# Performance work log

Hardware: AMD Instinct MI355X
Metric: run time of the kernel (lower is better)

The kernel has to match this reference:

```python
import jax, jax.numpy as jnp
import numpy as np

# ---- fixed sizes ----
N_IN = 100_000          # total inner nodes
NODES_PER_INNER = 50    # nodes per inner graph
N_OUT = N_IN // NODES_PER_INNER          # 2000 outer nodes (= num inner graphs)
NODES_PER_OUTER = 125   # outer nodes per outer graph
B = N_OUT // NODES_PER_OUTER             # 16 graphs in the batch
DEG = 8
E_IN = N_IN * DEG        # 800_000 inner edges
E_OUT = N_OUT * DEG      # 16_000 outer edges
IN_FEATS = 64
OUT_FEATS = 64
H = 128                  # h_feats = [128]*6
NUM_CLASSES = 10


def _rand_edges(key, n_graphs, nodes_per_graph, edges_per_graph):
    """Random edges that stay inside each graph of a batched graph."""
    k1, k2 = jax.random.split(key)
    src_l = jax.random.randint(k1, (n_graphs, edges_per_graph), 0, nodes_per_graph)
    dst_l = jax.random.randint(k2, (n_graphs, edges_per_graph), 0, nodes_per_graph)
    off = (jnp.arange(n_graphs) * nodes_per_graph)[:, None]
    return ((src_l + off).reshape(-1).astype(jnp.int32),
            (dst_l + off).reshape(-1).astype(jnp.int32))


def setup_inputs() -> dict:
    key = jax.random.key(0)
    ks = jax.random.split(key, 24)
    inner_src, inner_dst = _rand_edges(ks[0], N_OUT, NODES_PER_INNER, E_IN // N_OUT)
    outer_src, outer_dst = _rand_edges(ks[1], B, NODES_PER_OUTER, E_OUT // B)

    def w(k, fan_in, fan_out):
        return jax.random.normal(k, (fan_in, fan_out), jnp.float32) * (1.0 / np.sqrt(fan_in))

    inp = {
        "in_layer_feat": jax.random.normal(ks[2], (N_IN, IN_FEATS), jnp.float32),
        "out_layer_feat": jax.random.normal(ks[3], (N_OUT, OUT_FEATS), jnp.float32),
        "inner_ew": jax.random.uniform(ks[4], (E_IN,), jnp.float32) + 0.5,
        "outer_ew": jax.random.uniform(ks[5], (E_OUT,), jnp.float32) + 0.5,
        "W1": w(ks[6], IN_FEATS, H),        "b1": jnp.zeros((H,), jnp.float32),
        "W2": w(ks[7], H, H),               "b2": jnp.zeros((H,), jnp.float32),
        "W3": w(ks[8], OUT_FEATS + H, H),   "b3": jnp.zeros((H,), jnp.float32),
        "W4": w(ks[9], H, H),               "b4": jnp.zeros((H,), jnp.float32),
        "W5": w(ks[10], H, H),              "b5": jnp.zeros((H,), jnp.float32),
        "W6": w(ks[11], H, H),              "b6": jnp.zeros((H,), jnp.float32),
        "Wc": w(ks[12], H, NUM_CLASSES),    "bc": jnp.zeros((NUM_CLASSES,), jnp.float32),
        "inner_src": inner_src, "inner_dst": inner_dst,
        "outer_src": outer_src, "outer_dst": outer_dst,
        "inner_node_graph": (jnp.arange(N_IN) // NODES_PER_INNER).astype(jnp.int32),
        "outer_node_graph": (jnp.arange(N_OUT) // NODES_PER_OUTER).astype(jnp.int32),
    }
    return inp


def graph_conv(src, dst, ew, x, W, b, n_nodes):
    """DGL GraphConv, norm='both', weighted aggregation, zero-in-degree allowed."""
    ones = jnp.ones(src.shape[0], x.dtype)
    deg_out = jnp.clip(jax.ops.segment_sum(ones, src, num_segments=n_nodes), 1.0)
    deg_in = jnp.clip(jax.ops.segment_sum(ones, dst, num_segments=n_nodes), 1.0)
    xs = x * jax.lax.rsqrt(deg_out)[:, None]                      # src normalization
    msg = xs[src] * ew[:, None]                                   # u_mul_e
    agg = jax.ops.segment_sum(msg, dst, num_segments=n_nodes)     # copy_e -> sum
    agg = agg * jax.lax.rsqrt(deg_in)[:, None]                    # dst normalization
    return agg @ W + b


def mean_nodes(h, node_graph, n_graphs, nodes_per_graph):
    return jax.ops.segment_sum(h, node_graph, num_segments=n_graphs) / nodes_per_graph


def reference(in_layer_feat, out_layer_feat, inner_ew, outer_ew,
              W1, b1, W2, b2, W3, b3, W4, b4, W5, b5, W6, b6, Wc, bc,
              inner_src, inner_dst, outer_src, outer_dst,
              inner_node_graph, outer_node_graph):
    # inner-graph message passing
    h = jax.nn.relu(graph_conv(inner_src, inner_dst, inner_ew, in_layer_feat, W1, b1, N_IN))
    h = jax.nn.relu(graph_conv(inner_src, inner_dst, inner_ew, h, W2, b2, N_IN))
    reduced = mean_nodes(h, inner_node_graph, N_OUT, float(NODES_PER_INNER))  # [N_OUT, H]
    merged = jnp.concatenate([out_layer_feat, reduced], axis=-1)              # [N_OUT, OUT_FEATS+H]
    # outer-graph message passing
    h = jax.nn.relu(graph_conv(outer_src, outer_dst, outer_ew, merged, W3, b3, N_OUT))
    h = jax.nn.relu(graph_conv(outer_src, outer_dst, outer_ew, h, W4, b4, N_OUT))
    h = jax.nn.relu(graph_conv(outer_src, outer_dst, outer_ew, h, W5, b5, N_OUT))
    h = jax.nn.relu(graph_conv(outer_src, outer_dst, outer_ew, h, W6, b6, N_OUT))
    hg = mean_nodes(h, outer_node_graph, B, float(NODES_PER_OUTER))           # [B, H]
    return hg @ Wc + bc                                                       # [B, NUM_CLASSES]
```

## Files before the change

kernel.cpp:

```cpp
#include <hip/hip_runtime.h>

#define NPI 50
#define EPI 400
#define NPO 125
#define EPO 1000
#define N_IN 100000
#define N_OUT 2000
#define NB 16
#define NC 10

typedef _Float16 half_t;
typedef _Float16 f16x8 __attribute__((ext_vector_type(8)));
typedef float f32x4 __attribute__((ext_vector_type(4)));

#define MFMA(a, b, c) __builtin_amdgcn_mfma_f32_16x16x32_f16(a, b, c, 0, 0, 0)

__device__ __forceinline__ f16x8 lds_ld8(const half_t* base, int row, int k, int strideB) {
    return *(const f16x8*)((const char*)base + row * strideB + ((k * 2) ^ ((row & 7) << 4)));
}
__device__ __forceinline__ void lds_st1(half_t* base, int row, int col, int strideB, float v) {
    *(half_t*)((char*)base + row * strideB + ((col * 2) ^ ((row & 7) << 4))) = (half_t)v;
}
__device__ __forceinline__ void lds_st1h(half_t* base, int row, int col, int strideB, half_t v) {
    *(half_t*)((char*)base + row * strideB + ((col * 2) ^ ((row & 7) << 4))) = v;
}
__device__ __forceinline__ void lds_st8(half_t* base, int row, int k, int strideB, f16x8 v) {
    *(f16x8*)((char*)base + row * strideB + ((k * 2) ^ ((row & 7) << 4))) = v;
}
__device__ __forceinline__ f16x8 scr_ld8(const half_t* base, int row, int k) {
    return *(const f16x8*)((const char*)base + row * 64 + ((k * 2) ^ ((row & 3) << 4)));
}
__device__ __forceinline__ void scr_st1(half_t* base, int row, int col, float v) {
    *(half_t*)((char*)base + row * 64 + ((col * 2) ^ ((row & 3) << 4))) = (half_t)v;
}

__global__ __launch_bounds__(256) void k_pre(
    const float* __restrict__ W1, const float* __restrict__ W2,
    const float* __restrict__ W3, const float* __restrict__ W4,
    const float* __restrict__ W5, const float* __restrict__ W6,
    half_t* __restrict__ WT1, half_t* __restrict__ WT2,
    half_t* __restrict__ WT3, half_t* __restrict__ WT4,
    half_t* __restrict__ WT5, half_t* __restrict__ WT6,
    const float* __restrict__ ew, const int* __restrict__ esrc,
    const int* __restrict__ edst, half_t* __restrict__ Aout)
{
    __shared__ float Af[NPO * NPO];
    __shared__ int cO[NPO], cI[NPO];
    __shared__ float rso[NPO], rsi[NPO];
    const int t = threadIdx.x;

    if (blockIdx.x < 384) {
        int i = blockIdx.x * 256 + t;
        const float* src; half_t* dst; int K;
        if      (i < 8192)  { src = W1; dst = WT1; K = 64; }
        else if (i < 24576) { src = W2; dst = WT2; K = 128; i -= 8192; }
        else if (i < 49152) { src = W3; dst = WT3; K = 192; i -= 24576; }
        else if (i < 65536) { src = W4; dst = WT4; K = 128; i -= 49152; }
        else if (i < 81920) { src = W5; dst = WT5; K = 128; i -= 65536; }
        else                { src = W6; dst = WT6; K = 128; i -= 81920; }
        int c = i & 127, k = i >> 7;
        dst[c * K + k] = (half_t)src[k * 128 + c];
        return;
    }

    const int g = blockIdx.x - 384;
    const int nb = g * NPO, eb = g * EPO;
    for (int i = t; i < NPO * NPO; i += 256) Af[i] = 0.f;
    if (t < NPO) { cO[t] = 0; cI[t] = 0; }
    __syncthreads();
    for (int e = t; e < EPO; e += 256) {
        int s = esrc[eb + e] - nb, d = edst[eb + e] - nb;
        atomicAdd(&Af[d * NPO + s], ew[eb + e]);
        atomicAdd(&cO[s], 1); atomicAdd(&cI[d], 1);
    }
    __syncthreads();
    if (t < NPO) {
        rso[t] = rsqrtf((float)max(cO[t], 1));
        rsi[t] = rsqrtf((float)max(cI[t], 1));
    }
    __syncthreads();
    for (int i = t; i < 128 * 16; i += 256) {
        int d = i >> 4, s0 = (i & 15) * 8;
        f16x8 v;
        #pragma unroll
        for (int j = 0; j < 8; j++) {
            int s = s0 + j;
            float x = (d < NPO && s < NPO) ? Af[d * NPO + s] * rsi[d] * rso[s] : 0.f;
            v[j] = (half_t)x;
        }
        *(f16x8*)&Aout[(size_t)g * 16384 + d * 128 + s0] = v;
    }
}

__global__ __launch_bounds__(256, 7) void k_inner(
    const float* __restrict__ X, const float* __restrict__ outfeat,
    const float* __restrict__ ew, const int* __restrict__ esrc,
    const int* __restrict__ edst,
    const half_t* __restrict__ WT1, const float* __restrict__ b1,
    const half_t* __restrict__ WT2, const float* __restrict__ b2,
    half_t* __restrict__ merged)
{
    __shared__ alignas(16) char smem[21504];
    half_t* R2  = (half_t*)smem;
    float*  Af  = (float*)smem;
    half_t* scr = (half_t*)(smem + 16384);
    float*  pool= (float*)(smem + 20480);
    int*    cO  = (int*)(smem + 20992);
    int*    cI  = (int*)(smem + 21248);

    const int g = blockIdx.x, t = threadIdx.x;
    const int w = t >> 6, l = t & 63, lr = l & 15, lk = l >> 4;
    const int nb = g * NPI, eb = g * EPI;
    half_t* scrw = scr + w * 512;

    float ofv = (t < 64) ? outfeat[(size_t)g * 64 + t] : 0.f;
    int s0e, d0e; float w0e;
    { int e = eb + t; s0e = esrc[e] - nb; d0e = edst[e] - nb; w0e = ew[e]; }
    int s1e = 0, d1e = 0; float w1e = 0.f;
    const bool e1v = (t + 256 < EPI);
    if (e1v) { int e = eb + t + 256; s1e = esrc[e] - nb; d1e = edst[e] - nb; w1e = ew[e]; }
    const int srow = t >> 2, qc = t & 3;
    float4 xr0 = {0,0,0,0}, xr1 = xr0, xr2 = xr0, xr3 = xr0;
    if (srow < NPI) {
        const float* xp = &X[(size_t)(nb + srow) * 64 + qc * 16];
        xr0 = *(const float4*)(xp + 0);
        xr1 = *(const float4*)(xp + 4);
        xr2 = *(const float4*)(xp + 8);
        xr3 = *(const float4*)(xp + 12);
    }

    if (t < 64) { cO[t] = 0; cI[t] = 0; }
    if (t >= 64 && t < 192) pool[t - 64] = 0.f;
    for (int i = t; i < 4096; i += 256) Af[i] = 0.f;
    __syncthreads();

    atomicAdd(&Af[d0e * 64 + (s0e ^ ((d0e & 7) << 2))], w0e);
    atomicAdd(&cO[s0e], 1); atomicAdd(&cI[d0e], 1);
    if (e1v) {
        atomicAdd(&Af[d1e * 64 + (s1e ^ ((d1e & 7) << 2))], w1e);
        atomicAdd(&cO[s1e], 1); atomicAdd(&cI[d1e], 1);
    }
    __syncthreads();

    f16x8 afr[2];
    {
        const int r = w * 16 + lr;
        const int sw = (r & 7) << 2;
        const float rsi_l = rsqrtf((float)max(cI[r], 1));
        #pragma unroll
        for (int ks = 0; ks < 2; ks++) {
            const int c0 = ks * 32 + lk * 8;
            f32x4 v0 = *(const f32x4*)&Af[r * 64 + (c0 ^ sw)];
            f32x4 v1 = *(const f32x4*)&Af[r * 64 + ((c0 + 4) ^ sw)];
            f16x8 fr;
            #pragma unroll
            for (int j = 0; j < 4; j++)
                fr[j] = (half_t)(v0[j] * rsi_l * rsqrtf((float)max(cO[c0 + j], 1)));
            #pragma unroll
            for (int j = 0; j < 4; j++)
                fr[4 + j] = (half_t)(v1[j] * rsi_l * rsqrtf((float)max(cO[c0 + 4 + j], 1)));
            afr[ks] = fr;
        }
    }
    __syncthreads();

    {
        float xv[16] = {xr0.x,xr0.y,xr0.z,xr0.w, xr1.x,xr1.y,xr1.z,xr1.w,
                        xr2.x,xr2.y,xr2.z,xr2.w, xr3.x,xr3.y,xr3.z,xr3.w};
        #pragma unroll
        for (int i = 0; i < 16; i++) lds_st1(R2, qc * 16 + i, srow, 128, xv[i]);
    }
    __syncthreads();

    f32x4 hacc[8] = {};
    #pragma unroll
    for (int kf = 0; kf < 2; kf++) {
        #pragma unroll
        for (int j = 0; j < 2; j++) {
            const int ft = kf * 2 + j;
            f32x4 tacc = {};
            #pragma unroll
            for (int ks = 0; ks < 2; ks++) {
                f16x8 b = lds_ld8(R2, ft * 16 + lr, ks * 32 + lk * 8, 128);
                tacc = MFMA(afr[ks], b, tacc);
            }
            #pragma unroll
            for (int q = 0; q < 4; q++) scr_st1(scrw, lk * 4 + q, j * 16 + lr, tacc[q]);
        }
        f16x8 a1 = scr_ld8(scrw, lr, lk * 8);
        #pragma unroll
        for (int nt = 0; nt < 8; nt++) {
            f16x8 b = *(const f16x8*)&WT1[(nt * 16 + lr) * 64 + kf * 32 + lk * 8];
            hacc[nt] = MFMA(a1, b, hacc[nt]);
        }
    }
    __syncthreads();
    #pragma unroll
    for (int nt = 0; nt < 8; nt++) {
        int c = nt * 16 + lr;
        float bb = b1[c];
        #pragma unroll
        for (int q = 0; q < 4; q++)
            lds_st1(R2, c, w * 16 + lk * 4 + q, 128, fmaxf(hacc[nt][q] + bb, 0.f));
    }
    __syncthreads();

    f32x4 h2[8] = {};
    #pragma unroll
    for (int kf = 0; kf < 4; kf++) {
        #pragma unroll
        for (int j = 0; j < 2; j++) {
            const int ft = kf * 2 + j;
            f32x4 tacc = {};
            #pragma unroll
            for (int ks = 0; ks < 2; ks++) {
                f16x8 b = lds_ld8(R2, ft * 16 + lr, ks * 32 + lk * 8, 128);
                tacc = MFMA(afr[ks], b, tacc);
            }
            #pragma unroll
            for (int q = 0; q < 4; q++) scr_st1(scrw, lk * 4 + q, j * 16 + lr, tacc[q]);
        }
        f16x8 a1 = scr_ld8(scrw, lr, lk * 8);
        #pragma unroll
        for (int nt = 0; nt < 8; nt++) {
            f16x8 b = *(const f16x8*)&WT2[(nt * 16 + lr) * 128 + kf * 32 + lk * 8];
            h2[nt] = MFMA(a1, b, h2[nt]);
        }
    }
    #pragma unroll
    for (int nt = 0; nt < 8; nt++) {
        int c = nt * 16 + lr;
        float bb = b2[c];
        float ps = 0.f;
        #pragma unroll
        for (int q = 0; q < 4; q++) {
            int m = w * 16 + lk * 4 + q;
            float v = fmaxf(h2[nt][q] + bb, 0.f);
            ps += (m < NPI) ? v : 0.f;
        }
        ps += __shfl_xor(ps, 16);
        ps += __shfl_xor(ps, 32);
        if (lk == 0) atomicAdd(&pool[c], ps);
    }
    __syncthreads();
    if (t < 64) merged[(size_t)g * 192 + t] = (half_t)ofv;
    else if (t < 192) merged[(size_t)g * 192 + t] = (half_t)(pool[t - 64] * (1.f / NPI));
}

template <int FIN, bool STAGE, bool LAST>
__device__ __forceinline__ void outer_layer(
    const half_t* AgL, const half_t* __restrict__ mg,
    const half_t* __restrict__ WT, const float* __restrict__ bias,
    half_t* bufP, half_t* bufQ, float* pool,
    int w, int lr, int lk, int t)
{
    f32x4 hacc[8] = {};
    constexpr int NCH = FIN / 64;
    #pragma unroll
    for (int ch = 0; ch < NCH; ch++) {
        if constexpr (STAGE) {
            __syncthreads();
            for (int i = t; i < 1024; i += 512) {
                int s = i >> 3, fo = (i & 7) * 8;
                f16x8 hv = {};
                if (s < NPO) hv = *(const f16x8*)&mg[(size_t)s * 192 + ch * 64 + fo];
                #pragma unroll
                for (int j = 0; j < 8; j++) lds_st1h(bufP, fo + j, s, 256, hv[j]);
            }
            __syncthreads();
        }
        const int rb = STAGE ? 0 : ch * 64;
        f32x4 tacc[4] = {};
        #pragma unroll
        for (int ks = 0; ks < 4; ks++) {
            f16x8 a = lds_ld8(AgL, w * 16 + lr, ks * 32 + lk * 8, 256);
            #pragma unroll
            for (int nt = 0; nt < 4; nt++) {
                f16x8 b = lds_ld8(bufP, rb + nt * 16 + lr, ks * 32 + lk * 8, 256);
                tacc[nt] = MFMA(a, b, tacc[nt]);
            }
        }
        #pragma unroll
        for (int nt = 0; nt < 4; nt++)
            #pragma unroll
            for (int q = 0; q < 4; q++)
                lds_st1(bufQ, w * 16 + lk * 4 + q, nt * 16 + lr, 128, tacc[nt][q]);
        #pragma unroll
        for (int ks2 = 0; ks2 < 2; ks2++) {
            f16x8 a1 = lds_ld8(bufQ, w * 16 + lr, ks2 * 32 + lk * 8, 128);
            #pragma unroll
            for (int nt = 0; nt < 8; nt++) {
                f16x8 b = *(const f16x8*)&WT[(nt * 16 + lr) * FIN + ch * 64 + ks2 * 32 + lk * 8];
                hacc[nt] = MFMA(a1, b, hacc[nt]);
            }
        }
    }
    __syncthreads();
    if constexpr (!LAST) {
        #pragma unroll
        for (int nt = 0; nt < 8; nt++) {
            int c = nt * 16 + lr;
            float bb = bias[c];
            #pragma unroll
            for (int q = 0; q < 4; q++)
                lds_st1(bufP, c, w * 16 + lk * 4 + q, 256, fmaxf(hacc[nt][q] + bb, 0.f));
        }
        __syncthreads();
    } else {
        #pragma unroll
        for (int nt = 0; nt < 8; nt++) {
            int c = nt * 16 + lr;
            float bb = bias[c];
            float ps = 0.f;
            #pragma unroll
            for (int q = 0; q < 4; q++) {
                int d = w * 16 + lk * 4 + q;
                float v = fmaxf(hacc[nt][q] + bb, 0.f);
                ps += (d < NPO) ? v : 0.f;
            }
            ps += __shfl_xor(ps, 16);
            ps += __shfl_xor(ps, 32);
            if (lk == 0) atomicAdd(&pool[c], ps);
        }
        __syncthreads();
    }
}

__global__ __launch_bounds__(512) void k_outer(
    const half_t* __restrict__ Aout, const half_t* __restrict__ merged,
    const half_t* __restrict__ WT3, const float* __restrict__ b3,
    const half_t* __restrict__ WT4, const float* __restrict__ b4,
    const half_t* __restrict__ WT5, const float* __restrict__ b5,
    const half_t* __restrict__ WT6, const float* __restrict__ b6,
    const float* __restrict__ Wc, const float* __restrict__ bc,
    float* __restrict__ out)
{
    __shared__ alignas(16) char smem[82432];
    half_t* AgL  = (half_t*)smem;
    half_t* bufP = (half_t*)(smem + 32768);
    half_t* bufQ = (half_t*)(smem + 65536);
    float*  pool = (float*)(smem + 81920);

    const int g = blockIdx.x, t = threadIdx.x;
    const int w = t >> 6, l = t & 63, lr = l & 15, lk = l >> 4;
    const half_t* mg = merged + (size_t)g * NPO * 192;

    for (int i = t; i < 2048; i += 512) {
        int row = i >> 4, k0 = (i & 15) * 8;
        f16x8 v = *(const f16x8*)&Aout[(size_t)g * 16384 + row * 128 + k0];
        lds_st8(AgL, row, k0, 256, v);
    }
    if (t < 128) pool[t] = 0.f;
    __syncthreads();

    outer_layer<192, true,  false>(AgL, mg, WT3, b3, bufP, bufQ, pool, w, lr, lk, t);
    outer_layer<128, false, false>(AgL, nullptr, WT4, b4, bufP, bufQ, pool, w, lr, lk, t);
    outer_layer<128, false, false>(AgL, nullptr, WT5, b5, bufP, bufQ, pool, w, lr, lk, t);
    outer_layer<128, false, true >(AgL, nullptr, WT6, b6, bufP, bufQ, pool, w, lr, lk, t);

    if (t < NC) {
        float acc = bc[t];
        for (int k = 0; k < 128; k++)
            acc = fmaf(pool[k] * (1.f / NPO), Wc[k * NC + t], acc);
        out[g * NC + t] = acc;
    }
}

extern "C" void kernel_launch(void* const* d_in, const int* in_sizes, int n_in,
                              void* d_out, int out_size, void* d_ws, size_t ws_size,
                              hipStream_t stream)
{
    const float* X       = (const float*)d_in[0];
    const float* outfeat = (const float*)d_in[1];
    const float* iew     = (const float*)d_in[2];
    const float* oew     = (const float*)d_in[3];
    const float* W1 = (const float*)d_in[4];  const float* b1 = (const float*)d_in[5];
    const float* W2 = (const float*)d_in[6];  const float* b2 = (const float*)d_in[7];
    const float* W3 = (const float*)d_in[8];  const float* b3 = (const float*)d_in[9];
    const float* W4 = (const float*)d_in[10]; const float* b4 = (const float*)d_in[11];
    const float* W5 = (const float*)d_in[12]; const float* b5 = (const float*)d_in[13];
    const float* W6 = (const float*)d_in[14]; const float* b6 = (const float*)d_in[15];
    const float* Wc = (const float*)d_in[16]; const float* bc = (const float*)d_in[17];
    const int* isrc = (const int*)d_in[18];   const int* idst = (const int*)d_in[19];
    const int* osrc = (const int*)d_in[20];   const int* odst = (const int*)d_in[21];

    char* base = (char*)d_ws;
    half_t* WT1 = (half_t*)(base + 0);
    half_t* WT2 = (half_t*)(base + 16384);
    half_t* WT3 = (half_t*)(base + 49152);
    half_t* WT4 = (half_t*)(base + 98304);
    half_t* WT5 = (half_t*)(base + 131072);
    half_t* WT6 = (half_t*)(base + 163840);
    half_t* AoutG  = (half_t*)(base + 196608);
    half_t* merged = (half_t*)(base + 720896);

    k_pre<<<400, 256, 0, stream>>>(W1, W2, W3, W4, W5, W6,
                                   WT1, WT2, WT3, WT4, WT5, WT6,
                                   oew, osrc, odst, AoutG);
    k_inner<<<N_OUT, 256, 0, stream>>>(X, outfeat, iew, isrc, idst,
                                       WT1, b1, WT2, b2, merged);
    k_outer<<<NB, 512, 0, stream>>>(AoutG, merged, WT3, b3, WT4, b4,
                                    WT5, b5, WT6, b6, Wc, bc, (float*)d_out);
}
```

Measured before the change: 141.4 us.

## Double outer-kernel threads, keep adjacency in registers, prefetch weights in both kernels

After: 122.3 us. -13.5%, faster.

```diff
diff --git a/kernel.cpp b/kernel.cpp
--- a/kernel.cpp
+++ b/kernel.cpp
@@ -23,9 +23,6 @@
 }
 __device__ __forceinline__ void lds_st1h(half_t* base, int row, int col, int strideB, half_t v) {
     *(half_t*)((char*)base + row * strideB + ((col * 2) ^ ((row & 7) << 4))) = v;
-}
-__device__ __forceinline__ void lds_st8(half_t* base, int row, int k, int strideB, f16x8 v) {
-    *(f16x8*)((char*)base + row * strideB + ((k * 2) ^ ((row & 7) << 4))) = v;
 }
 __device__ __forceinline__ f16x8 scr_ld8(const half_t* base, int row, int k) {
     return *(const f16x8*)((const char*)base + row * 64 + ((k * 2) ^ ((row & 3) << 4)));
@@ -92,7 +89,7 @@
     }
 }
 
-__global__ __launch_bounds__(256, 7) void k_inner(
+__global__ __launch_bounds__(256, 5) void k_inner(
     const float* __restrict__ X, const float* __restrict__ outfeat,
     const float* __restrict__ ew, const int* __restrict__ esrc,
     const int* __restrict__ edst,
@@ -120,13 +117,15 @@
     const bool e1v = (t + 256 < EPI);
     if (e1v) { int e = eb + t + 256; s1e = esrc[e] - nb; d1e = edst[e] - nb; w1e = ew[e]; }
     const int srow = t >> 2, qc = t & 3;
-    float4 xr0 = {0,0,0,0}, xr1 = xr0, xr2 = xr0, xr3 = xr0;
+    f16x8 xh0 = {}, xh1 = {};
     if (srow < NPI) {
         const float* xp = &X[(size_t)(nb + srow) * 64 + qc * 16];
-        xr0 = *(const float4*)(xp + 0);
-        xr1 = *(const float4*)(xp + 4);
-        xr2 = *(const float4*)(xp + 8);
-        xr3 = *(const float4*)(xp + 12);
+        float4 a = *(const float4*)(xp + 0), b = *(const float4*)(xp + 4);
+        float4 c = *(const float4*)(xp + 8), d = *(const float4*)(xp + 12);
+        xh0[0]=(half_t)a.x; xh0[1]=(half_t)a.y; xh0[2]=(half_t)a.z; xh0[3]=(half_t)a.w;
+        xh0[4]=(half_t)b.x; xh0[5]=(half_t)b.y; xh0[6]=(half_t)b.z; xh0[7]=(half_t)b.w;
+        xh1[0]=(half_t)c.x; xh1[1]=(half_t)c.y; xh1[2]=(half_t)c.z; xh1[3]=(half_t)c.w;
+        xh1[4]=(half_t)d.x; xh1[5]=(half_t)d.y; xh1[6]=(half_t)d.z; xh1[7]=(half_t)d.w;
     }
 
     if (t < 64) { cO[t] = 0; cI[t] = 0; }
@@ -164,17 +163,19 @@
     }
     __syncthreads();
 
-    {
-        float xv[16] = {xr0.x,xr0.y,xr0.z,xr0.w, xr1.x,xr1.y,xr1.z,xr1.w,
-                        xr2.x,xr2.y,xr2.z,xr2.w, xr3.x,xr3.y,xr3.z,xr3.w};
-        #pragma unroll
-        for (int i = 0; i < 16; i++) lds_st1(R2, qc * 16 + i, srow, 128, xv[i]);
-    }
+    #pragma unroll
+    for (int i = 0; i < 8; i++) lds_st1h(R2, qc * 16 + i, srow, 128, xh0[i]);
+    #pragma unroll
+    for (int i = 0; i < 8; i++) lds_st1h(R2, qc * 16 + 8 + i, srow, 128, xh1[i]);
     __syncthreads();
 
     f32x4 hacc[8] = {};
     #pragma unroll
     for (int kf = 0; kf < 2; kf++) {
+        f16x8 wb[8];
+        #pragma unroll
+        for (int nt = 0; nt < 8; nt++)
+            wb[nt] = *(const f16x8*)&WT1[(nt * 16 + lr) * 64 + kf * 32 + lk * 8];
         #pragma unroll
         for (int j = 0; j < 2; j++) {
             const int ft = kf * 2 + j;
@@ -189,10 +190,7 @@
         }
         f16x8 a1 = scr_ld8(scrw, lr, lk * 8);
         #pragma unroll
-        for (int nt = 0; nt < 8; nt++) {
-            f16x8 b = *(const f16x8*)&WT1[(nt * 16 + lr) * 64 + kf * 32 + lk * 8];
-            hacc[nt] = MFMA(a1, b, hacc[nt]);
-        }
+        for (int nt = 0; nt < 8; nt++) hacc[nt] = MFMA(a1, wb[nt], hacc[nt]);
     }
     __syncthreads();
     #pragma unroll
@@ -208,6 +206,10 @@
     f32x4 h2[8] = {};
     #pragma unroll
     for (int kf = 0; kf < 4; kf++) {
+        f16x8 wb[8];
+        #pragma unroll
+        for (int nt = 0; nt < 8; nt++)
+            wb[nt] = *(const f16x8*)&WT2[(nt * 16 + lr) * 128 + kf * 32 + lk * 8];
         #pragma unroll
         for (int j = 0; j < 2; j++) {
             const int ft = kf * 2 + j;
@@ -222,10 +224,7 @@
         }
         f16x8 a1 = scr_ld8(scrw, lr, lk * 8);
         #pragma unroll
-        for (int nt = 0; nt < 8; nt++) {
-            f16x8 b = *(const f16x8*)&WT2[(nt * 16 + lr) * 128 + kf * 32 + lk * 8];
-            h2[nt] = MFMA(a1, b, h2[nt]);
-        }
+        for (int nt = 0; nt < 8; nt++) h2[nt] = MFMA(a1, wb[nt], h2[nt]);
     }
     #pragma unroll
     for (int nt = 0; nt < 8; nt++) {
@@ -249,72 +248,82 @@
 
 template <int FIN, bool STAGE, bool LAST>
 __device__ __forceinline__ void outer_layer(
-    const half_t* AgL, const half_t* __restrict__ mg,
+    const f16x8* afr, const half_t* __restrict__ mg,
     const half_t* __restrict__ WT, const float* __restrict__ bias,
     half_t* bufP, half_t* bufQ, float* pool,
-    int w, int lr, int lk, int t)
+    int wr, int wc, int lr, int lk, int t)
 {
-    f32x4 hacc[8] = {};
+    f32x4 hacc[4] = {};
     constexpr int NCH = FIN / 64;
+    f16x8 hv[NCH];
+    if constexpr (STAGE) {
+        const int s = t >> 3, fo = (t & 7) * 8;
+        #pragma unroll
+        for (int ch = 0; ch < NCH; ch++) {
+            f16x8 z = {};
+            hv[ch] = (s < NPO) ? *(const f16x8*)&mg[(size_t)s * 192 + ch * 64 + fo] : z;
+        }
+    }
     #pragma unroll
     for (int ch = 0; ch < NCH; ch++) {
+        f16x8 wtb[8];
+        #pragma unroll
+        for (int ks2 = 0; ks2 < 2; ks2++)
+            #pragma unroll
+            for (int nt = 0; nt < 4; nt++)
+                wtb[ks2 * 4 + nt] = *(const f16x8*)&WT[
+                    (size_t)(wc * 64 + nt * 16 + lr) * FIN + ch * 64 + ks2 * 32 + lk * 8];
         if constexpr (STAGE) {
+            const int s = t >> 3, fo = (t & 7) * 8;
+            #pragma unroll
+            for (int j = 0; j < 8; j++) lds_st1h(bufP, fo + j, s, 256, hv[ch][j]);
             __syncthreads();
-            for (int i = t; i < 1024; i += 512) {
-                int s = i >> 3, fo = (i & 7) * 8;
-                f16x8 hv = {};
-                if (s < NPO) hv = *(const f16x8*)&mg[(size_t)s * 192 + ch * 64 + fo];
-                #pragma unroll
-                for (int j = 0; j < 8; j++) lds_st1h(bufP, fo + j, s, 256, hv[j]);
+        }
+        const int rb = STAGE ? 0 : ch * 64;
+        f32x4 tacc[2] = {};
+        #pragma unroll
+        for (int ks = 0; ks < 4; ks++) {
+            #pragma unroll
+            for (int nt = 0; nt < 2; nt++) {
+                f16x8 b = lds_ld8(bufP, rb + wc * 32 + nt * 16 + lr, ks * 32 + lk * 8, 256);
+                tacc[nt] = MFMA(afr[ks], b, tacc[nt]);
             }
-            __syncthreads();
-        }
-        const int rb = STAGE ? 0 : ch * 64;
-        f32x4 tacc[4] = {};
-        #pragma unroll
-        for (int ks = 0; ks < 4; ks++) {
-            f16x8 a = lds_ld8(AgL, w * 16 + lr, ks * 32 + lk * 8, 256);
-            #pragma unroll
-            for (int nt = 0; nt < 4; nt++) {
-                f16x8 b = lds_ld8(bufP, rb + nt * 16 + lr, ks * 32 + lk * 8, 256);
-                tacc[nt] = MFMA(a, b, tacc[nt]);
-            }
-        }
-        #pragma unroll
-        for (int nt = 0; nt < 4; nt++)
+        }
+        #pragma unroll
+        for (int nt = 0; nt < 2; nt++)
             #pragma unroll
             for (int q = 0; q < 4; q++)
-                lds_st1(bufQ, w * 16 + lk * 4 + q, nt * 16 + lr, 128, tacc[nt][q]);
+                lds_st1(bufQ, wr * 16 + lk * 4 + q, wc * 32 + nt * 16 + lr, 128,
+                        tacc[nt][q]);
+        __syncthreads();
         #pragma unroll
         for (int ks2 = 0; ks2 < 2; ks2++) {
-            f16x8 a1 = lds_ld8(bufQ, w * 16 + lr, ks2 * 32 + lk * 8, 128);
-            #pragma unroll
-            for (int nt = 0; nt < 8; nt++) {
-                f16x8 b = *(const f16x8*)&WT[(nt * 16 + lr) * FIN + ch * 64 + ks2 * 32 + lk * 8];
-                hacc[nt] = MFMA(a1, b, hacc[nt]);
-            }
-        }
-    }
-    __syncthreads();
+            f16x8 a1 = lds_ld8(bufQ, wr * 16 + lr, ks2 * 32 + lk * 8, 128);
+            #pragma unroll
+            for (int nt = 0; nt < 4; nt++)
+                hacc[nt] = MFMA(a1, wtb[ks2 * 4 + nt], hacc[nt]);
+        }
+        __syncthreads();
+    }
     if constexpr (!LAST) {
         #pragma unroll
-        for (int nt = 0; nt < 8; nt++) {
-            int c = nt * 16 + lr;
+        for (int nt = 0; nt < 4; nt++) {
+            int c = wc * 64 + nt * 16 + lr;
             float bb = bias[c];
             #pragma unroll
             for (int q = 0; q < 4; q++)
-                lds_st1(bufP, c, w * 16 + lk * 4 + q, 256, fmaxf(hacc[nt][q] + bb, 0.f));
+                lds_st1(bufP, c, wr * 16 + lk * 4 + q, 256, fmaxf(hacc[nt][q] + bb, 0.f));
         }
         __syncthreads();
     } else {
         #pragma unroll
-        for (int nt = 0; nt < 8; nt++) {
-            int c = nt * 16 + lr;
+        for (int nt = 0; nt < 4; nt++) {
+            int c = wc * 64 + nt * 16 + lr;
             float bb = bias[c];
             float ps = 0.f;
             #pragma unroll
             for (int q = 0; q < 4; q++) {
-                int d = w * 16 + lk * 4 + q;
+                int d = wr * 16 + lk * 4 + q;
                 float v = fmaxf(hacc[nt][q] + bb, 0.f);
                 ps += (d < NPO) ? v : 0.f;
             }
@@ -326,7 +335,7 @@
     }
 }
 
-__global__ __launch_bounds__(512) void k_outer(
+__global__ __launch_bounds__(1024) void k_outer(
     const half_t* __restrict__ Aout, const half_t* __restrict__ merged,
     const half_t* __restrict__ WT3, const float* __restrict__ b3,
     const half_t* __restrict__ WT4, const float* __restrict__ b4,
@@ -335,35 +344,46 @@
     const float* __restrict__ Wc, const float* __restrict__ bc,
     float* __restrict__ out)
 {
-    __shared__ alignas(16) char smem[82432];
-    half_t* AgL  = (half_t*)smem;
-    half_t* bufP = (half_t*)(smem + 32768);
-    half_t* bufQ = (half_t*)(smem + 65536);
-    float*  pool = (float*)(smem + 81920);
+    __shared__ alignas(16) char smem[49704];
+    half_t* bufP = (half_t*)smem;
+    half_t* bufQ = (half_t*)(smem + 32768);
+    float*  pool = (float*)(smem + 49152);
+    float*  cls  = (float*)(smem + 49664);
 
     const int g = blockIdx.x, t = threadIdx.x;
     const int w = t >> 6, l = t & 63, lr = l & 15, lk = l >> 4;
+    const int wr = w & 7, wc = w >> 3;
     const half_t* mg = merged + (size_t)g * NPO * 192;
 
-    for (int i = t; i < 2048; i += 512) {
-        int row = i >> 4, k0 = (i & 15) * 8;
-        f16x8 v = *(const f16x8*)&Aout[(size_t)g * 16384 + row * 128 + k0];
-        lds_st8(AgL, row, k0, 256, v);
-    }
+    f16x8 afr[4];
+    #pragma unroll
+    for (int ks = 0; ks < 4; ks++)
+        afr[ks] = *(const f16x8*)&Aout[(size_t)g * 16384
+                                       + (wr * 16 + lr) * 128 + ks * 32 + lk * 8];
     if (t < 128) pool[t] = 0.f;
-    __syncthreads();
-
-    outer_layer<192, true,  false>(AgL, mg, WT3, b3, bufP, bufQ, pool, w, lr, lk, t);
-    outer_layer<128, false, false>(AgL, nullptr, WT4, b4, bufP, bufQ, pool, w, lr, lk, t);
-    outer_layer<128, false, false>(AgL, nullptr, WT5, b5, bufP, bufQ, pool, w, lr, lk, t);
-    outer_layer<128, false, true >(AgL, nullptr, WT6, b6, bufP, bufQ, pool, w, lr, lk, t);
-
-    if (t < NC) {
-        float acc = bc[t];
-        for (int k = 0; k < 128; k++)
-            acc = fmaf(pool[k] * (1.f / NPO), Wc[k * NC + t], acc);
-        out[g * NC + t] = acc;
-    }
+    if (t >= 128 && t < 128 + NC) cls[t - 128] = 0.f;
+    __syncthreads();
+
+    outer_layer<192, true,  false>(afr, mg, WT3, b3, bufP, bufQ, pool, wr, wc, lr, lk, t);
+    outer_layer<128, false, false>(afr, nullptr, WT4, b4, bufP, bufQ, pool, wr, wc, lr, lk, t);
+    outer_layer<128, false, false>(afr, nullptr, WT5, b5, bufP, bufQ, pool, wr, wc, lr, lk, t);
+    outer_layer<128, false, true >(afr, nullptr, WT6, b6, bufP, bufQ, pool, wr, wc, lr, lk, t);
+
+    if (t < 128) {
+        float val = pool[t] * (1.f / NPO);
+        float p[NC];
+        #pragma unroll
+        for (int c = 0; c < NC; c++) p[c] = val * Wc[t * NC + c];
+        #pragma unroll
+        for (int off = 32; off >= 1; off >>= 1)
+            #pragma unroll
+            for (int c = 0; c < NC; c++) p[c] += __shfl_xor(p[c], off);
+        if ((t & 63) == 0)
+            #pragma unroll
+            for (int c = 0; c < NC; c++) atomicAdd(&cls[c], p[c]);
+    }
+    __syncthreads();
+    if (t < NC) out[g * NC + t] = cls[t] + bc[t];
 }
 
 extern "C" void kernel_launch(void* const* d_in, const int* in_sizes, int n_in,
@@ -399,6 +419,6 @@
                                    oew, osrc, odst, AoutG);
     k_inner<<<N_OUT, 256, 0, stream>>>(X, outfeat, iew, isrc, idst,
                                        WT1, b1, WT2, b2, merged);
-    k_outer<<<NB, 512, 0, stream>>>(AoutG, merged, WT3, b3, WT4, b4,
-                                    WT5, b5, WT6, b6, Wc, bc, (float*)d_out);
-}
+    k_outer<<<NB, 1024, 0, stream>>>(AoutG, merged, WT3, b3, WT4, b4,
+                                     WT5, b5, WT6, b6, Wc, bc, (float*)d_out);
+}
```
